# Kernel tuning notes

Measured on AMD Instinct MI355X. Metric: run time of the kernel, lower is better.

The kernel has to match this reference:

```python
import jax, jax.numpy as jnp
import numpy as np

N, L, K = 2048, 256, 16

def setup_inputs() -> dict:
    rng = np.random.default_rng(0)
    # per level: wavelet index = l (distinct across levels), plus K-1 random distinct rest indices
    sel = np.zeros((L, K), dtype=np.int64)
    wav = np.arange(L, dtype=np.int64)
    all_idx = np.arange(N)
    for l in range(L):
        others = rng.choice(np.delete(all_idx, l), size=K - 1, replace=False)
        sel[l] = np.sort(np.concatenate([[l], others]))
    key = jax.random.key(0)
    k1, k2 = jax.random.split(key)
    M = jax.random.normal(k1, (N, N), dtype=jnp.float32)
    A = 0.5 * (M + M.T)  # symmetric matrix, as MMF expects
    O_all = jax.random.normal(k2, (L, K, K), dtype=jnp.float32) / np.float32(K) ** 0.5
    return {"A": A, "O_all": O_all, "sel_idx": jnp.asarray(sel), "wav_idx": jnp.asarray(wav)}


def reference(A, O_all, sel_idx, wav_idx):
    # Torch builds a dense NxN U = eye with O scattered into the KxK block at
    # sel_idx x sel_idx, then A <- U A U^T and right <- U @ right.
    # Equivalent efficient form: only the K selected rows/cols change.
    n = A.shape[0]

    def step(carry, xs):
        A, right = carry
        O, idx = xs  # O: (K,K), idx: (K,)
        A = A.at[idx].set(O @ A[idx])              # U @ A   : rewrite K rows
        A = A.at[:, idx].set(A[:, idx] @ O.T)      # ... @ U^T: rewrite K cols
        right = right.at[idx].set(O @ right[idx])  # right <- U @ right
        return (A, right), None

    right0 = jnp.eye(n, dtype=A.dtype)
    (A_f, right), _ = jax.lax.scan(step, (A, right0), (O_all, sel_idx))

    # final_active_index: 1 everywhere except wavelet indices
    active = jnp.ones((n,), dtype=A.dtype).at[wav_idx].set(0.0)
    # left_index = eye - diag(diag(outer)) + outer  -> diag all ones, off-diag = a_i*a_j
    left = jnp.outer(active, active)
    left = left.at[jnp.diag_indices(n)].set(1.0)
    D = A_f * left
    A_rec = right.T @ D @ right
    return (A_rec, right, D)
```

## Files before the change

### kernel.cpp

```cpp
#include <hip/hip_runtime.h>

#define N 2048
#define LEV 256
#define KS 16

typedef __attribute__((ext_vector_type(8))) short bfx8;
typedef __attribute__((ext_vector_type(4))) float fx4;
typedef unsigned short u16;
typedef unsigned int u32;

static const size_t NN = (size_t)N * N;

__device__ inline u16 bf16_rne(float f) {
    u32 u = __builtin_bit_cast(u32, f);
    u32 r = (u + 0x7FFFu + ((u >> 16) & 1u)) >> 16;
    return (u16)r;
}
__device__ inline float bf16_f(u16 h) {
    u32 u = ((u32)h) << 16;
    return __builtin_bit_cast(float, u);
}

#define GLDS16(gp, lp) __builtin_amdgcn_global_load_lds( \
    (const __attribute__((address_space(1))) void*)(uintptr_t)(gp), \
    (__attribute__((address_space(3))) void*)(u32)(uintptr_t)(lp), 16, 0, 0)

__device__ inline float qadd(float x) {
#if __has_builtin(__builtin_amdgcn_mov_dpp)
    int a = __builtin_amdgcn_mov_dpp(__builtin_bit_cast(int, x), 0xB1, 0xF, 0xF, true);
    float y = x + __builtin_bit_cast(float, a);
    int b = __builtin_amdgcn_mov_dpp(__builtin_bit_cast(int, y), 0x4E, 0xF, 0xF, true);
    return y + __builtin_bit_cast(float, b);
#else
    float y = x + __shfl_xor(x, 1);
    return y + __shfl_xor(y, 2);
#endif
}

__global__ __launch_bounds__(64)
void build_right_k(const float* __restrict__ O_all, const int* __restrict__ sel,
                   float* __restrict__ RT) {
    __shared__ float x[2048];
    const int lane = threadIdx.x;
    const int i    = lane >> 2;
    const int kg   = lane & 3;
    const int col  = blockIdx.x;

    const float4 z = make_float4(0.f, 0.f, 0.f, 0.f);
    #pragma unroll
    for (int q = 0; q < 8; ++q) *(float4*)&x[q * 256 + lane * 4] = z;
    if (lane == 0) x[col] = 1.0f;

    const float* obase = O_all + i * KS + kg * 4;
    const int*   gbase = sel + kg * 4;

#define CMP(f, g, wv) { \
    float p = f.x * x[g.x] + f.y * x[g.y] + f.z * x[g.z] + f.w * x[g.w]; \
    p = qadd(p); \
    if (kg == 0) x[wv] = p; }

    float4 f0 = *(const float4*)(obase);
    int4   g0 = *(const int4*)(gbase);
    int    w0 = sel[i];
    float4 f1 = *(const float4*)(obase + 256);
    int4   g1 = *(const int4*)(gbase + KS);
    int    w1 = sel[KS + i];

    for (int l = 0; l < LEV; l += 2) {
        float4 f2, f3; int4 g2, g3; int w2, w3;
        if (l + 2 < LEV) {
            f2 = *(const float4*)(obase + (size_t)(l + 2) * 256);
            g2 = *(const int4*)(gbase + (l + 2) * KS);
            w2 = sel[(l + 2) * KS + i];
            f3 = *(const float4*)(obase + (size_t)(l + 3) * 256);
            g3 = *(const int4*)(gbase + (l + 3) * KS);
            w3 = sel[(l + 3) * KS + i];
        } else { f2 = f0; g2 = g0; w2 = w0; f3 = f1; g3 = g1; w3 = w1; }

        CMP(f0, g0, w0)
        CMP(f1, g1, w1)
        f0 = f2; g0 = g2; w0 = w2;
        f1 = f3; g1 = g3; w1 = w3;
    }
#undef CMP

    #pragma unroll
    for (int q = 0; q < 8; ++q)
        *(float4*)&RT[(size_t)col * N + q * 256 + lane * 4] =
            *(const float4*)&x[q * 256 + lane * 4];
}

__global__ __launch_bounds__(256)
void split_plain_k(const float* __restrict__ src, u16* __restrict__ dh) {
    u16* dl = dh + NN;
    size_t p = ((size_t)blockIdx.x * 256 + threadIdx.x) * 8;
    float4 v0 = *(const float4*)(src + p);
    float4 v1 = *(const float4*)(src + p + 4);
    float vv[8] = {v0.x, v0.y, v0.z, v0.w, v1.x, v1.y, v1.z, v1.w};
    bfx8 hs, ls;
    #pragma unroll
    for (int i = 0; i < 8; ++i) {
        u16 h = bf16_rne(vv[i]);
        hs[i] = (short)h;
        ls[i] = (short)bf16_rne(vv[i] - bf16_f(h));
    }
    *(bfx8*)(dh + p) = hs;
    *(bfx8*)(dl + p) = ls;
}

__global__ __launch_bounds__(256)
void split_rt_k(const float* __restrict__ RT, u16* __restrict__ r2h,
                u16* __restrict__ rth, float* __restrict__ Rrm) {
    __shared__ float t[64][65];
    u16* r2l = r2h + NN;
    u16* rtl = rth + NN;
    const int r0 = (blockIdx.x >> 5) * 64, c0 = (blockIdx.x & 31) * 64;
    #pragma unroll
    for (int i = 0; i < 16; ++i) {
        int q = i * 256 + threadIdx.x;
        int rr = q >> 6, cc = q & 63;
        t[rr][cc] = RT[(size_t)(r0 + rr) * N + c0 + cc];
    }
    __syncthreads();
    #pragma unroll
    for (int i = 0; i < 16; ++i) {
        int q = i * 256 + threadIdx.x;
        int rr = q >> 6, cc = q & 63;
        float v = t[rr][cc];
        u16 h = bf16_rne(v);
        size_t po = (size_t)(r0 + rr) * N + c0 + cc;
        rth[po] = h;
        rtl[po] = bf16_rne(v - bf16_f(h));
        float w = t[cc][rr];
        u16 h2 = bf16_rne(w);
        size_t pt = (size_t)(c0 + rr) * N + r0 + cc;
        r2h[pt] = h2;
        r2l[pt] = bf16_rne(w - bf16_f(h2));
        Rrm[pt] = w;
    }
}

__global__ __launch_bounds__(256)
void unsplit_k(const u16* __restrict__ hi, float* __restrict__ dst) {
    const u16* lo = hi + NN;
    size_t p = ((size_t)blockIdx.x * 256 + threadIdx.x) * 8;
    bfx8 hs = *(const bfx8*)(hi + p);
    bfx8 ls = *(const bfx8*)(lo + p);
    float4 o0, o1;
    o0.x = bf16_f((u16)hs[0]) + bf16_f((u16)ls[0]);
    o0.y = bf16_f((u16)hs[1]) + bf16_f((u16)ls[1]);
    o0.z = bf16_f((u16)hs[2]) + bf16_f((u16)ls[2]);
    o0.w = bf16_f((u16)hs[3]) + bf16_f((u16)ls[3]);
    o1.x = bf16_f((u16)hs[4]) + bf16_f((u16)ls[4]);
    o1.y = bf16_f((u16)hs[5]) + bf16_f((u16)ls[5]);
    o1.z = bf16_f((u16)hs[6]) + bf16_f((u16)ls[6]);
    o1.w = bf16_f((u16)hs[7]) + bf16_f((u16)ls[7]);
    *(float4*)(dst + p)     = o0;
    *(float4*)(dst + p + 4) = o1;
}

template<int MASKED, int OMODE, int SYNCV>
__global__ __launch_bounds__(256)
void gemm_bf3(const u16* __restrict__ Xp, const u16* __restrict__ Yp,
              float* __restrict__ Cf, u16* __restrict__ Cs,
              const int* __restrict__ wav, int Lw) {
    __shared__ __align__(16) u16 sm[2][4][8192];
    __shared__ float rowf[128], colf[128];

    const int tid = threadIdx.x;
    const int swz = ((blockIdx.x & 7) << 5) | (blockIdx.x >> 3);
    const int bx = swz & 15;
    const int by = swz >> 4;
    const int i0 = by * 128, j0 = bx * 128;
    const int lane = tid & 63, w = tid >> 6;
    const int wm = (w >> 1) * 64, wn = (w & 1) * 64;
    const int fr = lane & 15;

    if (MASKED) {
        if (tid < 128) rowf[tid] = 1.0f; else colf[tid - 128] = 1.0f;
        __syncthreads();
        for (int t = tid; t < Lw; t += 256) {
            int wv = wav[t];
            int dr = wv - i0; if (0 <= dr && dr < 128) rowf[dr] = 0.0f;
            int dc = wv - j0; if (0 <= dc && dc < 128) colf[dc] = 0.0f;
        }
    }

    fx4 acc[4][4];
    #pragma unroll
    for (int m = 0; m < 4; ++m)
        #pragma unroll
        for (int n = 0; n < 4; ++n)
            acc[m][n] = (fx4)0.0f;

    const u16* Xh = Xp; const u16* Xl = Xp + NN;
    const u16* Yh = Yp; const u16* Yl = Yp + NN;

    const int rl   = lane >> 3;
    const int gcol = ((lane & 7) ^ rl) << 3;
    const int wq   = w * 1024;

    #define STAGE(buf, kt) { \
        const int k0s = (kt) * 64; \
        char* lb0 = (char*)&sm[buf][0][0] + wq; \
        _Pragma("unroll") \
        for (int q = 0; q < 4; ++q) { \
            const int row = q * 32 + w * 8 + rl; \
            const size_t xo = (size_t)(i0 + row) * N + k0s + gcol; \
            const size_t yo = (size_t)(j0 + row) * N + k0s + gcol; \
            GLDS16(Xh + xo, lb0 + q * 4096); \
            GLDS16(Xl + xo, lb0 + 16384 + q * 4096); \
            GLDS16(Yh + yo, lb0 + 32768 + q * 4096); \
            GLDS16(Yl + yo, lb0 + 49152 + q * 4096); \
        } }

    const int kq  = (lane >> 4) << 4;
    const int frx = (fr & 7) << 4;

    #define COMPUTE(buf) { \
        const char* base = (const char*)&sm[buf][0][0]; \
        _Pragma("unroll") \
        for (int s = 0; s < 2; ++s) { \
            const int cb = s * 64 + kq; \
            bfx8 ah[4], al[4]; \
            _Pragma("unroll") \
            for (int m = 0; m < 4; ++m) { \
                const int off = (wm + m * 16 + fr) * 128 + (cb ^ frx); \
                ah[m] = *(const bfx8*)(base + off); \
                al[m] = *(const bfx8*)(base + 16384 + off); \
            } \
            _Pragma("unroll") \
            for (int n = 0; n < 4; ++n) { \
                const int off = (wn + n * 16 + fr) * 128 + (cb ^ frx); \
                bfx8 bh = *(const bfx8*)(base + 32768 + off); \
                bfx8 bl = *(const bfx8*)(base + 49152 + off); \
                _Pragma("unroll") \
                for (int m = 0; m < 4; ++m) { \
                    acc[m][n] = __builtin_amdgcn_mfma_f32_16x16x32_bf16(ah[m], bh, acc[m][n], 0, 0, 0); \
                    acc[m][n] = __builtin_amdgcn_mfma_f32_16x16x32_bf16(ah[m], bl, acc[m][n], 0, 0, 0); \
                    acc[m][n] = __builtin_amdgcn_mfma_f32_16x16x32_bf16(al[m], bh, acc[m][n], 0, 0, 0); \
                } \
            } \
        } }

    constexpr int NT = N / 64;
    STAGE(0, 0)
    if (SYNCV == 0) {
        __syncthreads();
        for (int kt = 0; kt < NT; ++kt) {
            const int cur = kt & 1;
            if (kt + 1 < NT) STAGE(cur ^ 1, kt + 1)
            COMPUTE(cur)
            __syncthreads();
        }
    } else {
        for (int kt = 0; kt < NT; ++kt) {
            const int cur = kt & 1;
            if (kt + 1 < NT) {
                STAGE(cur ^ 1, kt + 1)
                asm volatile("s_waitcnt vmcnt(16)" ::: "memory");
            } else {
                asm volatile("s_waitcnt vmcnt(0)" ::: "memory");
            }
            __builtin_amdgcn_sched_barrier(0);
            __builtin_amdgcn_s_barrier();
            __builtin_amdgcn_sched_barrier(0);
            COMPUTE(cur)
            __builtin_amdgcn_sched_barrier(0);
            __builtin_amdgcn_s_barrier();
            __builtin_amdgcn_sched_barrier(0);
        }
    }

    const int crow0 = (lane >> 4) * 4;
    #pragma unroll
    for (int m = 0; m < 4; ++m) {
        #pragma unroll
        for (int n = 0; n < 4; ++n) {
            #pragma unroll
            for (int r = 0; r < 4; ++r) {
                const int li = wm + m * 16 + crow0 + r;
                const int lj = wn + n * 16 + fr;
                float v = acc[m][n][r];
                if (MASKED) {
                    if (i0 + li != j0 + lj) v *= rowf[li] * colf[lj];
                }
                const size_t off = (size_t)(i0 + li) * N + j0 + lj;
                if (OMODE == 0) {
                    Cf[off] = v;
                } else {
                    u16 h = bf16_rne(v);
                    Cs[off]      = h;
                    Cs[NN + off] = bf16_rne(v - bf16_f(h));
                }
            }
        }
    }
    #undef STAGE
    #undef COMPUTE
}

extern "C" void kernel_launch(void* const* d_in, const int* in_sizes, int n_in,
                              void* d_out, int out_size, void* d_ws, size_t ws_size,
                              hipStream_t stream) {
    const float* A     = (const float*)d_in[0];
    const float* O_all = (const float*)d_in[1];
    const int*   sel   = (const int*)d_in[2];
    const int*   wav   = (const int*)d_in[3];
    const int    Lw    = in_sizes[3];

    float* O1 = (float*)d_out;
    float* O2 = O1 + NN;
    float* O3 = O1 + 2 * NN;

    u16*   W1u = (u16*)d_ws;
    u16*   W2u = (u16*)((char*)d_ws + 2 * NN * sizeof(u16));
    u16*   O1u = (u16*)O1;
    u16*   O3u = (u16*)O3;

    const int SGRID = (int)(NN / (256 * 8));

    split_plain_k<<<SGRID, 256, 0, stream>>>(A, W2u);
    build_right_k<<<N, 64, 0, stream>>>(O_all, sel, O3);
    split_rt_k<<<(N / 64) * (N / 64), 256, 0, stream>>>(O3, O1u, W1u, O2);

    gemm_bf3<0, 1, 0><<<256, 256, 0, stream>>>(O1u, W2u, nullptr, O3u, nullptr, 0);
    gemm_bf3<1, 1, 0><<<256, 256, 0, stream>>>(O3u, O1u, nullptr, W2u, wav, Lw);
    gemm_bf3<0, 1, 1><<<256, 256, 0, stream>>>(W1u, W2u, nullptr, O3u, nullptr, 0);
    gemm_bf3<0, 0, 0><<<256, 256, 0, stream>>>(O3u, W1u, O1, nullptr, nullptr, 0);
    unsplit_k<<<SGRID, 256, 0, stream>>>(W2u, O3);
}
```

Before: 298.3 us.

## Process two columns per block in build_right and remap GEMM tiles per XCD

build_right_k now computes two columns of the rotation product per 64-thread block, sharing the O and index loads across both and halving the block count. The GEMM block-to-tile mapping changes from a plain XCD swizzle to grouping 4x4 super-tiles per XCD, aiming for better L2 reuse of the A and B panels. The manual vmcnt/s_barrier synchronisation variant is removed, so all GEMMs use the plain __syncthreads double-buffer loop. Doubling shared memory and work per block in build_right lowers its parallelism, and dropping the tuned sync path may lose overlap in one GEMM.

```diff
diff --git a/kernel.cpp b/kernel.cpp
--- a/kernel.cpp
+++ b/kernel.cpp
@@ -40,24 +40,28 @@
 __global__ __launch_bounds__(64)
 void build_right_k(const float* __restrict__ O_all, const int* __restrict__ sel,
                    float* __restrict__ RT) {
-    __shared__ float x[2048];
+    __shared__ float x[2][2052];
     const int lane = threadIdx.x;
     const int i    = lane >> 2;
     const int kg   = lane & 3;
-    const int col  = blockIdx.x;
+    const int col0 = blockIdx.x * 2;
 
     const float4 z = make_float4(0.f, 0.f, 0.f, 0.f);
     #pragma unroll
-    for (int q = 0; q < 8; ++q) *(float4*)&x[q * 256 + lane * 4] = z;
-    if (lane == 0) x[col] = 1.0f;
+    for (int q = 0; q < 8; ++q) {
+        *(float4*)&x[0][q * 256 + lane * 4] = z;
+        *(float4*)&x[1][q * 256 + lane * 4] = z;
+    }
+    if (lane < 2) x[lane][col0 + lane] = 1.0f;
 
     const float* obase = O_all + i * KS + kg * 4;
     const int*   gbase = sel + kg * 4;
 
 #define CMP(f, g, wv) { \
-    float p = f.x * x[g.x] + f.y * x[g.y] + f.z * x[g.z] + f.w * x[g.w]; \
-    p = qadd(p); \
-    if (kg == 0) x[wv] = p; }
+    float p0 = f.x * x[0][g.x] + f.y * x[0][g.y] + f.z * x[0][g.z] + f.w * x[0][g.w]; \
+    float p1 = f.x * x[1][g.x] + f.y * x[1][g.y] + f.z * x[1][g.z] + f.w * x[1][g.w]; \
+    p0 = qadd(p0); p1 = qadd(p1); \
+    if (kg == 0) { x[0][wv] = p0; x[1][wv] = p1; } }
 
     float4 f0 = *(const float4*)(obase);
     int4   g0 = *(const int4*)(gbase);
@@ -85,9 +89,11 @@
 #undef CMP
 
     #pragma unroll
-    for (int q = 0; q < 8; ++q)
-        *(float4*)&RT[(size_t)col * N + q * 256 + lane * 4] =
-            *(const float4*)&x[q * 256 + lane * 4];
+    for (int c = 0; c < 2; ++c)
+        #pragma unroll
+        for (int q = 0; q < 8; ++q)
+            *(float4*)&RT[(size_t)(col0 + c) * N + q * 256 + lane * 4] =
+                *(const float4*)&x[c][q * 256 + lane * 4];
 }
 
 __global__ __launch_bounds__(256)
@@ -159,7 +165,7 @@
     *(float4*)(dst + p + 4) = o1;
 }
 
-template<int MASKED, int OMODE, int SYNCV>
+template<int MASKED, int OMODE>
 __global__ __launch_bounds__(256)
 void gemm_bf3(const u16* __restrict__ Xp, const u16* __restrict__ Yp,
               float* __restrict__ Cf, u16* __restrict__ Cs,
@@ -168,9 +174,11 @@
     __shared__ float rowf[128], colf[128];
 
     const int tid = threadIdx.x;
-    const int swz = ((blockIdx.x & 7) << 5) | (blockIdx.x >> 3);
-    const int bx = swz & 15;
-    const int by = swz >> 4;
+    const int xcd = blockIdx.x & 7, idx = blockIdx.x >> 3;
+    const int sup = 2 * xcd + (idx >> 4);
+    const int wi4 = idx & 15;
+    const int by = ((sup >> 2) << 2) | (wi4 >> 2);
+    const int bx = ((sup & 3) << 2) | (wi4 & 3);
     const int i0 = by * 128, j0 = bx * 128;
     const int lane = tid & 63, w = tid >> 6;
     const int wm = (w >> 1) * 64, wn = (w & 1) * 64;
@@ -245,31 +253,12 @@
 
     constexpr int NT = N / 64;
     STAGE(0, 0)
-    if (SYNCV == 0) {
+    __syncthreads();
+    for (int kt = 0; kt < NT; ++kt) {
+        const int cur = kt & 1;
+        if (kt + 1 < NT) STAGE(cur ^ 1, kt + 1)
+        COMPUTE(cur)
         __syncthreads();
-        for (int kt = 0; kt < NT; ++kt) {
-            const int cur = kt & 1;
-            if (kt + 1 < NT) STAGE(cur ^ 1, kt + 1)
-            COMPUTE(cur)
-            __syncthreads();
-        }
-    } else {
-        for (int kt = 0; kt < NT; ++kt) {
-            const int cur = kt & 1;
-            if (kt + 1 < NT) {
-                STAGE(cur ^ 1, kt + 1)
-                asm volatile("s_waitcnt vmcnt(16)" ::: "memory");
-            } else {
-                asm volatile("s_waitcnt vmcnt(0)" ::: "memory");
-            }
-            __builtin_amdgcn_sched_barrier(0);
-            __builtin_amdgcn_s_barrier();
-            __builtin_amdgcn_sched_barrier(0);
-            COMPUTE(cur)
-            __builtin_amdgcn_sched_barrier(0);
-            __builtin_amdgcn_s_barrier();
-            __builtin_amdgcn_sched_barrier(0);
-        }
     }
 
     const int crow0 = (lane >> 4) * 4;
@@ -321,12 +310,12 @@
     const int SGRID = (int)(NN / (256 * 8));
 
     split_plain_k<<<SGRID, 256, 0, stream>>>(A, W2u);
-    build_right_k<<<N, 64, 0, stream>>>(O_all, sel, O3);
+    build_right_k<<<N / 2, 64, 0, stream>>>(O_all, sel, O3);
     split_rt_k<<<(N / 64) * (N / 64), 256, 0, stream>>>(O3, O1u, W1u, O2);
 
-    gemm_bf3<0, 1, 0><<<256, 256, 0, stream>>>(O1u, W2u, nullptr, O3u, nullptr, 0);
-    gemm_bf3<1, 1, 0><<<256, 256, 0, stream>>>(O3u, O1u, nullptr, W2u, wav, Lw);
-    gemm_bf3<0, 1, 1><<<256, 256, 0, stream>>>(W1u, W2u, nullptr, O3u, nullptr, 0);
-    gemm_bf3<0, 0, 0><<<256, 256, 0, stream>>>(O3u, W1u, O1, nullptr, nullptr, 0);
+    gemm_bf3<0, 1><<<256, 256, 0, stream>>>(O1u, W2u, nullptr, O3u, nullptr, 0);
+    gemm_bf3<1, 1><<<256, 256, 0, stream>>>(O3u, O1u, nullptr, W2u, wav, Lw);
+    gemm_bf3<0, 1><<<256, 256, 0, stream>>>(W1u, W2u, nullptr, O3u, nullptr, 0);
+    gemm_bf3<0, 0><<<256, 256, 0, stream>>>(O3u, W1u, O1, nullptr, nullptr, 0);
     unsplit_k<<<SGRID, 256, 0, stream>>>(W2u, O3);
 }
```

Result: faster. 290.4 us (-2.7%).
